# Optimization experiments

Measured on AMD Instinct MI355X. Metric: run time of the kernel, lower is better.

## Reference

```python
import jax, jax.numpy as jnp
import numpy as np

T, D, R, C, L = 4096, 512, 32, 32, 2  # time, input, trace, context, num_blocks
NEG_SLOPE = 0.01
EPS = 1e-5  # eqx LayerNorm default


def _layernorm(x, g, b):
    m = jnp.mean(x, -1, keepdims=True)
    v = jnp.var(x, -1, keepdims=True)
    return g * (x - m) * jax.lax.rsqrt(v + EPS) + b


def _ffa_scan(a, b, pre, s0, start):
    # a:[R], b:[C], pre:[T,R,C] real>=0, s0:[1,R,C] complex64, start:[T] bool
    ab = jax.lax.complex(jnp.broadcast_to(-jnp.abs(a)[:, None], (R, C)),
                         jnp.broadcast_to(b[None, :], (R, C)))  # log decay+rotation
    ts = jnp.concatenate([jnp.zeros((1,), jnp.float32), jnp.ones((T,), jnp.float32)])
    vals = jnp.concatenate([s0, pre.astype(jnp.complex64)], axis=0)  # [T+1,R,C]
    rst = jnp.concatenate([jnp.zeros((1,), bool), start])

    def op(l, r):
        tl, sl, dl = l
        tr, sr, dr = r
        decay = jnp.exp(ab[None, :, :] * tr[:, None, None])  # gamma^{t_r}
        s = jnp.where(dr[:, None, None], sr, sr + sl * decay)
        t = jnp.where(dr, tr, tl + tr)
        return (t, s, dl | dr)

    _, states, _ = jax.lax.associative_scan(op, (ts, vals, rst))
    return states[1:]  # [T,R,C]


def _forward(x, start_b, state_real, state_imag, Wt, Wc, a, b,
             W0, b0, g0, beta0, W1, b1, g1, beta1):
    h = x
    z = x
    for i in range(L):
        tr = h @ Wt[i].T  # [T,R]
        ct = h @ Wc[i].T  # [T,R] (source maps context proj to trace_size too; R==C)
        pre = jnp.abs(tr[:, :, None] * ct[:, None, :])  # [T,R,C] outer product
        pre = pre / (1e-8 + jnp.sum(pre, axis=(-2, -1), keepdims=True))
        s0 = jax.lax.complex(state_real[i], state_imag[i])  # [1,R,C]
        states = _ffa_scan(a[i], b[i], pre, s0, start_b)
        s = states.reshape(T, R * C)
        mag = jnp.log1p(jnp.abs(s))
        ang = jnp.angle(s)
        scaled = jnp.concatenate([mag * jnp.sin(ang), mag * jnp.cos(ang)], axis=-1)  # [T,2RC]
        z = jax.nn.leaky_relu(_layernorm(scaled @ W0[i].T + b0[i], g0[i], beta0[i]), NEG_SLOPE)
        z = jax.nn.leaky_relu(_layernorm(z @ W1[i].T + b1[i], g1[i], beta1[i]), NEG_SLOPE)
        h = h + z  # residual feeds next block; NSFFM returns last block's z
    return z


def setup_inputs() -> dict:
    key = jax.random.key(0)
    ks = jax.random.split(key, 8)
    x = jax.random.normal(ks[0], (T, D), jnp.float32)
    start = jax.random.randint(ks[1], (T,), 0, 2).astype(jnp.int32)
    next_done = jax.random.randint(ks[2], (T,), 0, 2).astype(jnp.int32)
    Wt = jax.random.normal(ks[3], (L, R, D), jnp.float32) / np.sqrt(D)
    Wc = jax.random.normal(ks[4], (L, R, D), jnp.float32) / np.sqrt(D)
    # ffa.init: a = linspace decays, b = log-spaced angular frequencies
    a = jnp.broadcast_to(jnp.linspace(1e-6, 0.5, R, dtype=jnp.float32)[None], (L, R)).copy()
    b = jnp.broadcast_to((2 * jnp.pi / jnp.exp(jnp.linspace(np.log(1.0), np.log(1024.0), C))).astype(jnp.float32)[None], (L, C)).copy()
    W0 = jax.random.normal(ks[5], (L, D, 2 * R * C), jnp.float32) * 0.01  # default_init scale=0.01
    W1 = jax.random.normal(ks[6], (L, D, D), jnp.float32) / np.sqrt(D)
    return {
        'x': x, 'start': start, 'next_done': next_done,
        'state_real': jnp.zeros((L, 1, R, C), jnp.float32),
        'state_imag': jnp.zeros((L, 1, R, C), jnp.float32),
        'Wt': Wt, 'Wc': Wc, 'a': a, 'b': b,
        'W0': W0, 'b0': jnp.zeros((L, D), jnp.float32),
        'g0': jnp.ones((L, D), jnp.float32), 'beta0': jnp.zeros((L, D), jnp.float32),
        'W1': W1, 'b1': jnp.zeros((L, D), jnp.float32),
        'g1': jnp.ones((L, D), jnp.float32), 'beta1': jnp.zeros((L, D), jnp.float32),
    }


def reference(x, start, next_done, state_real, state_imag, Wt, Wc, a, b,
              W0, b0, g0, beta0, W1, b1, g1, beta1):
    del next_done  # not used in the scan math (kept for interface parity)
    start_b = start.astype(bool)
    return _forward(x, start_b, state_real, state_imag, Wt, Wc, a, b,
                    W0, b0, g0, beta0, W1, b1, g1, beta1)
```

## Files before the change

kernel.cpp:

```cpp
#include <hip/hip_runtime.h>
#include <math.h>

#define TT 4096
#define DD 512
#define RR 32
#define CC 32
#define RC 1024
#define LL 2
#define CHUNK 32
#define NCHUNK 128
#define NEG_SLOPE 0.01f
#define LN_EPS 1e-5f

typedef __attribute__((ext_vector_type(8))) __bf16 bf16x8;
typedef __attribute__((ext_vector_type(4))) float f32x4;

__device__ __forceinline__ unsigned short f2bf(float f) {
    unsigned int u = __builtin_bit_cast(unsigned int, f);
    u += 0x7fffu + ((u >> 16) & 1u);
    return (unsigned short)(u >> 16);
}

#define NX4  524288
#define NW04 524288
#define NW14 131072
#define NCV  (NX4 + NW04 + NW14)
#define NPK  16384
__global__ __launch_bounds__(256) void setup_kernel(const float4* __restrict__ x,
                                                    const float4* __restrict__ W0,
                                                    const float4* __restrict__ W1,
                                                    const float* __restrict__ Wt,
                                                    const float* __restrict__ Wc,
                                                    ushort4* __restrict__ xb,
                                                    ushort4* __restrict__ W0b,
                                                    ushort4* __restrict__ W1b,
                                                    ushort4* __restrict__ Wtc) {
    int i = blockIdx.x * 256 + threadIdx.x;
    float4 v;
    ushort4* dst;
    int j;
    if (i < NCV) {
        const float4* src;
        if (i < NX4) { src = x; dst = xb; j = i; }
        else if (i < NX4 + NW04) { src = W0; dst = W0b; j = i - NX4; }
        else { src = W1; dst = W1b; j = i - NX4 - NW04; }
        v = src[j];
    } else {
        int ii = i - NCV;
        if (ii >= NPK) return;
        int e = ii * 4;
        int l = e >> 15;
        int r = (e >> 9) & 63;
        int k = e & 511;
        v = (r < 32) ? *(const float4*)&Wt[((size_t)l * 32 + r) * 512 + k]
                     : *(const float4*)&Wc[((size_t)l * 32 + (r - 32)) * 512 + k];
        dst = Wtc; j = ii;
    }
    ushort4 o;
    o.x = f2bf(v.x); o.y = f2bf(v.y); o.z = f2bf(v.z); o.w = f2bf(v.w);
    dst[j] = o;
}

__global__ __launch_bounds__(256) void proj_denom_kernel(const unsigned short* __restrict__ A,
                                                         const unsigned short* __restrict__ B,
                                                         float* __restrict__ tcabs) {
    __shared__ __align__(16) unsigned short As[128 * 32];
    __shared__ __align__(16) unsigned short Bs[64 * 32];
    __shared__ float sums[128][2];
    const int tid = threadIdx.x;
    const int w = tid >> 6, lane = tid & 63;
    const int bm = blockIdx.y * 128;
    const int wr = w >> 1, wc = w & 1;
    const int lr = lane >> 2;
    const int sl = lane & 3;
    const int swz_st = sl ^ ((lr >> 1) & 3);
    const int K = 512;
    const unsigned short* gA0 = A + (size_t)(bm + w * 16 + lr) * K + sl * 8;
    const unsigned short* gA1 = A + (size_t)(bm + 64 + w * 16 + lr) * K + sl * 8;
    const unsigned short* gB  = B + (size_t)(w * 16 + lr) * K + sl * 8;
    const int wA0 = (w * 16 + lr) * 32 + swz_st * 8;
    const int wA1 = (64 + w * 16 + lr) * 32 + swz_st * 8;
    const int wB  = (w * 16 + lr) * 32 + swz_st * 8;
    const int fr = lane & 15, hi = lane >> 4;
    const int kslot = hi ^ ((fr >> 1) & 3);
    f32x4 acc[4][2] = {};

    uint4 va0 = *(const uint4*)gA0;
    uint4 va1 = *(const uint4*)gA1;
    uint4 vb  = *(const uint4*)gB;
    for (int k0 = 0; k0 < K; k0 += 32) {
        __syncthreads();
        *(uint4*)&As[wA0] = va0;
        *(uint4*)&As[wA1] = va1;
        *(uint4*)&Bs[wB]  = vb;
        __syncthreads();
        if (k0 + 32 < K) {
            va0 = *(const uint4*)(gA0 + k0 + 32);
            va1 = *(const uint4*)(gA1 + k0 + 32);
            vb  = *(const uint4*)(gB  + k0 + 32);
        }
        bf16x8 af[4], bfv[2];
#pragma unroll
        for (int mi = 0; mi < 4; ++mi) {
            int row = wr * 64 + mi * 16 + fr;
            af[mi] = *(const bf16x8*)&As[row * 32 + kslot * 8];
        }
#pragma unroll
        for (int ni = 0; ni < 2; ++ni) {
            int row = wc * 32 + ni * 16 + fr;
            bfv[ni] = *(const bf16x8*)&Bs[row * 32 + kslot * 8];
        }
#pragma unroll
        for (int mi = 0; mi < 4; ++mi)
#pragma unroll
            for (int ni = 0; ni < 2; ++ni)
                acc[mi][ni] = __builtin_amdgcn_mfma_f32_16x16x32_bf16(
                    af[mi], bfv[ni], acc[mi][ni], 0, 0, 0);
    }
#pragma unroll
    for (int mi = 0; mi < 4; ++mi)
#pragma unroll
        for (int q = 0; q < 4; ++q) {
            float v = fabsf(acc[mi][0][q]) + fabsf(acc[mi][1][q]);
            v += __shfl_xor(v, 1);
            v += __shfl_xor(v, 2);
            v += __shfl_xor(v, 4);
            v += __shfl_xor(v, 8);
            if (fr == 0) sums[wr * 64 + mi * 16 + hi * 4 + q][wc] = v;
        }
    __syncthreads();
#pragma unroll
    for (int mi = 0; mi < 4; ++mi)
#pragma unroll
        for (int q = 0; q < 4; ++q) {
            int rl = wr * 64 + mi * 16 + hi * 4 + q;
            float inv = 1.f / (1e-8f + sums[rl][0] * sums[rl][1]);
            float scale = (wc == 0) ? inv : 1.f;
#pragma unroll
            for (int ni = 0; ni < 2; ++ni) {
                int col = wc * 32 + ni * 16 + fr;
                tcabs[(size_t)(bm + rl) * 64 + col] = fabsf(acc[mi][ni][q]) * scale;
            }
        }
}

__global__ __launch_bounds__(256) void scan_pass1(const float* __restrict__ tcabs,
                                                  const int* __restrict__ start,
                                                  const float* __restrict__ a,
                                                  const float* __restrict__ b,
                                                  float4* __restrict__ ab4) {
    int tid = blockIdx.x * 256 + threadIdx.x;
    int rc = tid & (RC - 1);
    int chunk = tid >> 10;
    int r = rc >> 5, c = rc & 31;
    float e = expf(-fabsf(a[r]));
    float gr = e * cosf(b[c]);
    float gi = e * sinf(b[c]);
    float alr = 1.f, ali = 0.f, ber = 0.f, bei = 0.f;
    int t0 = chunk * CHUNK;
    for (int j = 0; j < CHUNK; ++j) {
        int t = t0 + j;
        float pre = tcabs[t * 64 + r] * tcabs[t * 64 + 32 + c];
        if (start[t]) {
            alr = 0.f; ali = 0.f; ber = pre; bei = 0.f;
        } else {
            float nbr = pre + gr * ber - gi * bei;
            float nbi =       gr * bei + gi * ber;
            float nar = gr * alr - gi * ali;
            float nai = gr * ali + gi * alr;
            ber = nbr; bei = nbi; alr = nar; ali = nai;
        }
    }
    ab4[chunk * RC + rc] = make_float4(alr, ali, ber, bei);
}

__global__ __launch_bounds__(256) void scan_pass2f(const float* __restrict__ tcabs,
                                                   const float4* __restrict__ ab4,
                                                   const int* __restrict__ start,
                                                   const float* __restrict__ a,
                                                   const float* __restrict__ b,
                                                   const float* __restrict__ s0r,
                                                   const float* __restrict__ s0i,
                                                   unsigned short* __restrict__ scaled) {
    int bx = blockIdx.x;
    int chunk = bx >> 2;
    int rc = (bx & 3) * 256 + threadIdx.x;
    int r = rc >> 5, c = rc & 31;
    float e = expf(-fabsf(a[r]));
    float gr = e * cosf(b[c]);
    float gi = e * sinf(b[c]);
    float sr = s0r[rc], si = s0i[rc];
    int j = 0;
    for (; j + 8 <= chunk; j += 8) {
        float4 buf[8];
#pragma unroll
        for (int u = 0; u < 8; ++u) buf[u] = ab4[(j + u) * RC + rc];
#pragma unroll
        for (int u = 0; u < 8; ++u) {
            float nsr = buf[u].z + buf[u].x * sr - buf[u].y * si;
            float nsi = buf[u].w + buf[u].x * si + buf[u].y * sr;
            sr = nsr; si = nsi;
        }
    }
    for (; j < chunk; ++j) {
        float4 ab = ab4[j * RC + rc];
        float nsr = ab.z + ab.x * sr - ab.y * si;
        float nsi = ab.w + ab.x * si + ab.y * sr;
        sr = nsr; si = nsi;
    }
    int t0 = chunk * CHUNK;
    for (int jj = 0; jj < CHUNK; ++jj) {
        int t = t0 + jj;
        float pre = tcabs[t * 64 + r] * tcabs[t * 64 + 32 + c];
        if (start[t]) {
            sr = pre; si = 0.f;
        } else {
            float nsr = pre + gr * sr - gi * si;
            float nsi =       gr * si + gi * sr;
            sr = nsr; si = nsi;
        }
        float m = sqrtf(sr * sr + si * si);
        float mag = log1pf(m);
        float f = (m > 0.f) ? (mag / m) : 0.f;
        scaled[(size_t)t * 2048 + rc]        = f2bf(si * f);
        scaled[(size_t)t * 2048 + 1024 + rc] = f2bf(sr * f);
    }
}

template <int K, int N, int SPLITK>
__global__ __launch_bounds__(256) void gemm_bt_mfma(const unsigned short* __restrict__ A,
                                                    const unsigned short* __restrict__ B,
                                                    float* __restrict__ Cm) {
    __shared__ __align__(16) unsigned short As[128 * 32];
    __shared__ __align__(16) unsigned short Bs[64 * 32];
    const int tid = threadIdx.x;
    const int w = tid >> 6, lane = tid & 63;
    const int bm = blockIdx.y * 128, bn = blockIdx.x * 64;
    const int kbeg = blockIdx.z * (K / SPLITK);
    const int kend = kbeg + (K / SPLITK);
    const int wr = w >> 1, wc = w & 1;
    const int lr = lane >> 2;
    const int sl = lane & 3;
    const int swz_st = sl ^ ((lr >> 1) & 3);
    const size_t a_row0 = (size_t)(bm + w * 16 + lr);
    const size_t a_row1 = (size_t)(bm + 64 + w * 16 + lr);
    const size_t b_row  = (size_t)(bn + w * 16 + lr);
    const unsigned short* gA0 = A + a_row0 * K + sl * 8;
    const unsigned short* gA1 = A + a_row1 * K + sl * 8;
    const unsigned short* gB  = B + b_row  * K + sl * 8;
    const int wA0 = (w * 16 + lr) * 32 + swz_st * 8;
    const int wA1 = (64 + w * 16 + lr) * 32 + swz_st * 8;
    const int wB  = (w * 16 + lr) * 32 + swz_st * 8;
    const int fr = lane & 15, hi = lane >> 4;
    const int kslot = hi ^ ((fr >> 1) & 3);
    f32x4 acc[4][2] = {};

    uint4 va0 = *(const uint4*)(gA0 + kbeg);
    uint4 va1 = *(const uint4*)(gA1 + kbeg);
    uint4 vb  = *(const uint4*)(gB  + kbeg);
    for (int k0 = kbeg; k0 < kend; k0 += 32) {
        __syncthreads();
        *(uint4*)&As[wA0] = va0;
        *(uint4*)&As[wA1] = va1;
        *(uint4*)&Bs[wB]  = vb;
        __syncthreads();
        if (k0 + 32 < kend) {
            va0 = *(const uint4*)(gA0 + k0 + 32);
            va1 = *(const uint4*)(gA1 + k0 + 32);
            vb  = *(const uint4*)(gB  + k0 + 32);
        }
        bf16x8 af[4], bfv[2];
#pragma unroll
        for (int mi = 0; mi < 4; ++mi) {
            int row = wr * 64 + mi * 16 + fr;
            af[mi] = *(const bf16x8*)&As[row * 32 + kslot * 8];
        }
#pragma unroll
        for (int ni = 0; ni < 2; ++ni) {
            int row = wc * 32 + ni * 16 + fr;
            bfv[ni] = *(const bf16x8*)&Bs[row * 32 + kslot * 8];
        }
#pragma unroll
        for (int mi = 0; mi < 4; ++mi)
#pragma unroll
            for (int ni = 0; ni < 2; ++ni)
                acc[mi][ni] = __builtin_amdgcn_mfma_f32_16x16x32_bf16(
                    af[mi], bfv[ni], acc[mi][ni], 0, 0, 0);
    }
    float* Cz = Cm + (size_t)blockIdx.z * TT * N;
    const int ccol0 = bn + wc * 32 + fr;
    const int crow0 = bm + wr * 64 + hi * 4;
#pragma unroll
    for (int ni = 0; ni < 2; ++ni) {
        int col = ccol0 + ni * 16;
#pragma unroll
        for (int mi = 0; mi < 4; ++mi)
#pragma unroll
            for (int q = 0; q < 4; ++q)
                Cz[(size_t)(crow0 + mi * 16 + q) * N + col] = acc[mi][ni][q];
    }
}

__global__ __launch_bounds__(256) void ln_lrelu_kernel(const float* __restrict__ y0,
                                                       const float* __restrict__ y1,
                                                       const float* __restrict__ badd,
                                                       const float* __restrict__ g,
                                                       const float* __restrict__ be,
                                                       unsigned short* __restrict__ zb,
                                                       const float* __restrict__ res,
                                                       unsigned short* __restrict__ hbf,
                                                       float* __restrict__ fout) {
    int t = blockIdx.x;
    int tid = threadIdx.x;
    size_t base = (size_t)t * 512;
    float v0 = y0[base + tid] + y1[base + tid] + badd[tid];
    float v1 = y0[base + 256 + tid] + y1[base + 256 + tid] + badd[256 + tid];
    float s = v0 + v1, ss = v0 * v0 + v1 * v1;
#pragma unroll
    for (int o = 32; o > 0; o >>= 1) {
        s  += __shfl_down(s, o);
        ss += __shfl_down(ss, o);
    }
    __shared__ float sh[8];
    __shared__ float mrs[2];
    int wid = tid >> 6, lane = tid & 63;
    if (lane == 0) { sh[wid] = s; sh[4 + wid] = ss; }
    __syncthreads();
    if (tid == 0) {
        float S = sh[0] + sh[1] + sh[2] + sh[3];
        float SS = sh[4] + sh[5] + sh[6] + sh[7];
        float m = S * (1.f / 512.f);
        float var = SS * (1.f / 512.f) - m * m;
        mrs[0] = m;
        mrs[1] = rsqrtf(var + LN_EPS);
    }
    __syncthreads();
    float m = mrs[0], rs = mrs[1];
    float z0 = g[tid] * (v0 - m) * rs + be[tid];
    float z1 = g[256 + tid] * (v1 - m) * rs + be[256 + tid];
    z0 = (z0 > 0.f) ? z0 : NEG_SLOPE * z0;
    z1 = (z1 > 0.f) ? z1 : NEG_SLOPE * z1;
    if (zb)   { zb[base + tid] = f2bf(z0); zb[base + 256 + tid] = f2bf(z1); }
    if (hbf) {
        float h0 = (res ? res[base + tid] : 0.f) + z0;
        float h1 = (res ? res[base + 256 + tid] : 0.f) + z1;
        hbf[base + tid] = f2bf(h0);
        hbf[base + 256 + tid] = f2bf(h1);
    }
    if (fout) { fout[base + tid] = z0; fout[base + 256 + tid] = z1; }
}

extern "C" void kernel_launch(void* const* d_in, const int* in_sizes, int n_in,
                              void* d_out, int out_size, void* d_ws, size_t ws_size,
                              hipStream_t stream) {
    const float* x     = (const float*)d_in[0];
    const int*   start = (const int*)d_in[1];
    const float* s0r = (const float*)d_in[3];
    const float* s0i = (const float*)d_in[4];
    const float* Wt  = (const float*)d_in[5];
    const float* Wc  = (const float*)d_in[6];
    const float* a   = (const float*)d_in[7];
    const float* b   = (const float*)d_in[8];
    const float* W0  = (const float*)d_in[9];
    const float* b0  = (const float*)d_in[10];
    const float* g0  = (const float*)d_in[11];
    const float* be0 = (const float*)d_in[12];
    const float* W1  = (const float*)d_in[13];
    const float* b1  = (const float*)d_in[14];
    const float* g1  = (const float*)d_in[15];
    const float* be1 = (const float*)d_in[16];
    float* out = (float*)d_out;
    float* ws  = (float*)d_ws;

    float* p = ws;
    float* tcabs  = p; p += 262144;
    float4* ab4   = (float4*)p; p += 524288;
    unsigned short* scaled = (unsigned short*)p; p += 4194304;
    float* ybufp  = p; p += 4194304;
    unsigned short* zbuf_bf = (unsigned short*)p; p += 1048576;
    unsigned short* x_bf    = (unsigned short*)p; p += 1048576;
    unsigned short* h_bf    = (unsigned short*)p; p += 1048576;
    unsigned short* Wtcbf   = (unsigned short*)p; p += 32768;
    unsigned short* W0bf    = (unsigned short*)p; p += 1048576;
    unsigned short* W1bf    = (unsigned short*)p; p += 262144;

    setup_kernel<<<(NCV + NPK + 255) / 256, 256, 0, stream>>>(
        (const float4*)x, (const float4*)W0, (const float4*)W1, Wt, Wc,
        (ushort4*)x_bf, (ushort4*)W0bf, (ushort4*)W1bf, (ushort4*)Wtcbf);

    for (int i = 0; i < LL; ++i) {
        const unsigned short* hb = (i == 0) ? x_bf : h_bf;
        proj_denom_kernel<<<dim3(1, 32), 256, 0, stream>>>(
            hb, Wtcbf + (size_t)i * 64 * 512, tcabs);
        scan_pass1<<<NCHUNK * RC / 256, 256, 0, stream>>>(
            tcabs, start, a + i * RR, b + i * CC, ab4);
        scan_pass2f<<<NCHUNK * 4, 256, 0, stream>>>(
            tcabs, ab4, start, a + i * RR, b + i * CC,
            s0r + i * RC, s0i + i * RC, scaled);
        gemm_bt_mfma<2048, 512, 2><<<dim3(8, 32, 2), 256, 0, stream>>>(
            scaled, W0bf + (size_t)i * 512 * 2048, ybufp);
        ln_lrelu_kernel<<<TT, 256, 0, stream>>>(
            ybufp, ybufp + (size_t)TT * 512, b0 + i * DD, g0 + i * DD, be0 + i * DD,
            zbuf_bf, nullptr, nullptr, nullptr);
        gemm_bt_mfma<512, 512, 2><<<dim3(8, 32, 2), 256, 0, stream>>>(
            zbuf_bf, W1bf + (size_t)i * 512 * 512, ybufp);
        ln_lrelu_kernel<<<TT, 256, 0, stream>>>(
            ybufp, ybufp + (size_t)TT * 512, b1 + i * DD, g1 + i * DD, be1 + i * DD,
            nullptr,
            (i < LL - 1) ? x : nullptr,
            (i < LL - 1) ? h_bf : nullptr,
            (i == LL - 1) ? out : nullptr);
    }
}
```

Baseline: 208.9 us.

## Retile projection kernel to 64-row blocks and remap GEMM workgroups across XCDs

The projection/denominator kernel now uses 64-row tiles with each wave owning 16 full rows, so it launches 64 workgroups instead of 32. The row normalizer is computed with in-wave shuffles alone, which removes the shared-memory sums array and an extra barrier. The main GEMM now remaps its linear workgroup id so that consecutive tiles land on the same XCD (8-way interleave), meant to improve L2 reuse of shared A/B tiles. This assumes the workgroup count is divisible by 8, and each wave in the projection kernel does less reuse of its A fragment.

```diff
diff --git a/kernel.cpp b/kernel.cpp
--- a/kernel.cpp
+++ b/kernel.cpp
@@ -64,84 +64,61 @@
 __global__ __launch_bounds__(256) void proj_denom_kernel(const unsigned short* __restrict__ A,
                                                          const unsigned short* __restrict__ B,
                                                          float* __restrict__ tcabs) {
-    __shared__ __align__(16) unsigned short As[128 * 32];
+    __shared__ __align__(16) unsigned short As[64 * 32];
     __shared__ __align__(16) unsigned short Bs[64 * 32];
-    __shared__ float sums[128][2];
     const int tid = threadIdx.x;
     const int w = tid >> 6, lane = tid & 63;
-    const int bm = blockIdx.y * 128;
-    const int wr = w >> 1, wc = w & 1;
-    const int lr = lane >> 2;
-    const int sl = lane & 3;
-    const int swz_st = sl ^ ((lr >> 1) & 3);
+    const int bm = blockIdx.x * 64;
     const int K = 512;
-    const unsigned short* gA0 = A + (size_t)(bm + w * 16 + lr) * K + sl * 8;
-    const unsigned short* gA1 = A + (size_t)(bm + 64 + w * 16 + lr) * K + sl * 8;
-    const unsigned short* gB  = B + (size_t)(w * 16 + lr) * K + sl * 8;
-    const int wA0 = (w * 16 + lr) * 32 + swz_st * 8;
-    const int wA1 = (64 + w * 16 + lr) * 32 + swz_st * 8;
-    const int wB  = (w * 16 + lr) * 32 + swz_st * 8;
+    const int srow = tid >> 2;
+    const int sl = tid & 3;
+    const int sswz = (sl ^ ((srow >> 1) & 3)) * 8;
+    const unsigned short* gA = A + (size_t)(bm + srow) * K + sl * 8;
+    const unsigned short* gB = B + (size_t)srow * K + sl * 8;
+    const int wA = srow * 32 + sswz;
+    const int wB = srow * 32 + sswz;
     const int fr = lane & 15, hi = lane >> 4;
     const int kslot = hi ^ ((fr >> 1) & 3);
-    f32x4 acc[4][2] = {};
-
-    uint4 va0 = *(const uint4*)gA0;
-    uint4 va1 = *(const uint4*)gA1;
-    uint4 vb  = *(const uint4*)gB;
+    f32x4 acc0 = {}, acc1 = {}, acc2 = {}, acc3 = {};
+
+    uint4 va = *(const uint4*)gA;
+    uint4 vb = *(const uint4*)gB;
     for (int k0 = 0; k0 < K; k0 += 32) {
         __syncthreads();
-        *(uint4*)&As[wA0] = va0;
-        *(uint4*)&As[wA1] = va1;
-        *(uint4*)&Bs[wB]  = vb;
+        *(uint4*)&As[wA] = va;
+        *(uint4*)&Bs[wB] = vb;
         __syncthreads();
         if (k0 + 32 < K) {
-            va0 = *(const uint4*)(gA0 + k0 + 32);
-            va1 = *(const uint4*)(gA1 + k0 + 32);
-            vb  = *(const uint4*)(gB  + k0 + 32);
-        }
-        bf16x8 af[4], bfv[2];
-#pragma unroll
-        for (int mi = 0; mi < 4; ++mi) {
-            int row = wr * 64 + mi * 16 + fr;
-            af[mi] = *(const bf16x8*)&As[row * 32 + kslot * 8];
-        }
-#pragma unroll
-        for (int ni = 0; ni < 2; ++ni) {
-            int row = wc * 32 + ni * 16 + fr;
-            bfv[ni] = *(const bf16x8*)&Bs[row * 32 + kslot * 8];
-        }
-#pragma unroll
-        for (int mi = 0; mi < 4; ++mi)
-#pragma unroll
-            for (int ni = 0; ni < 2; ++ni)
-                acc[mi][ni] = __builtin_amdgcn_mfma_f32_16x16x32_bf16(
-                    af[mi], bfv[ni], acc[mi][ni], 0, 0, 0);
-    }
-#pragma unroll
-    for (int mi = 0; mi < 4; ++mi)
-#pragma unroll
-        for (int q = 0; q < 4; ++q) {
-            float v = fabsf(acc[mi][0][q]) + fabsf(acc[mi][1][q]);
-            v += __shfl_xor(v, 1);
-            v += __shfl_xor(v, 2);
-            v += __shfl_xor(v, 4);
-            v += __shfl_xor(v, 8);
-            if (fr == 0) sums[wr * 64 + mi * 16 + hi * 4 + q][wc] = v;
-        }
-    __syncthreads();
-#pragma unroll
-    for (int mi = 0; mi < 4; ++mi)
-#pragma unroll
-        for (int q = 0; q < 4; ++q) {
-            int rl = wr * 64 + mi * 16 + hi * 4 + q;
-            float inv = 1.f / (1e-8f + sums[rl][0] * sums[rl][1]);
-            float scale = (wc == 0) ? inv : 1.f;
-#pragma unroll
-            for (int ni = 0; ni < 2; ++ni) {
-                int col = wc * 32 + ni * 16 + fr;
-                tcabs[(size_t)(bm + rl) * 64 + col] = fabsf(acc[mi][ni][q]) * scale;
-            }
-        }
+            va = *(const uint4*)(gA + k0 + 32);
+            vb = *(const uint4*)(gB + k0 + 32);
+        }
+        const int arow = w * 16 + fr;
+        bf16x8 af = *(const bf16x8*)&As[arow * 32 + kslot * 8];
+        bf16x8 b0 = *(const bf16x8*)&Bs[(0 * 16 + fr) * 32 + kslot * 8];
+        bf16x8 b1 = *(const bf16x8*)&Bs[(1 * 16 + fr) * 32 + kslot * 8];
+        bf16x8 b2 = *(const bf16x8*)&Bs[(2 * 16 + fr) * 32 + kslot * 8];
+        bf16x8 b3 = *(const bf16x8*)&Bs[(3 * 16 + fr) * 32 + kslot * 8];
+        acc0 = __builtin_amdgcn_mfma_f32_16x16x32_bf16(af, b0, acc0, 0, 0, 0);
+        acc1 = __builtin_amdgcn_mfma_f32_16x16x32_bf16(af, b1, acc1, 0, 0, 0);
+        acc2 = __builtin_amdgcn_mfma_f32_16x16x32_bf16(af, b2, acc2, 0, 0, 0);
+        acc3 = __builtin_amdgcn_mfma_f32_16x16x32_bf16(af, b3, acc3, 0, 0, 0);
+    }
+#pragma unroll
+    for (int q = 0; q < 4; ++q) {
+        float a0 = fabsf(acc0[q]), a1 = fabsf(acc1[q]);
+        float a2 = fabsf(acc2[q]), a3 = fabsf(acc3[q]);
+        float st = a0 + a1, sc = a2 + a3;
+        st += __shfl_xor(st, 1); sc += __shfl_xor(sc, 1);
+        st += __shfl_xor(st, 2); sc += __shfl_xor(sc, 2);
+        st += __shfl_xor(st, 4); sc += __shfl_xor(sc, 4);
+        st += __shfl_xor(st, 8); sc += __shfl_xor(sc, 8);
+        float inv = 1.f / (1e-8f + st * sc);
+        size_t rb = (size_t)(bm + w * 16 + hi * 4 + q) * 64;
+        tcabs[rb + fr]      = a0 * inv;
+        tcabs[rb + fr + 16] = a1 * inv;
+        tcabs[rb + fr + 32] = a2;
+        tcabs[rb + fr + 48] = a3;
+    }
 }
 
 __global__ __launch_bounds__(256) void scan_pass1(const float* __restrict__ tcabs,
@@ -235,8 +212,15 @@
     __shared__ __align__(16) unsigned short Bs[64 * 32];
     const int tid = threadIdx.x;
     const int w = tid >> 6, lane = tid & 63;
-    const int bm = blockIdx.y * 128, bn = blockIdx.x * 64;
-    const int kbeg = blockIdx.z * (K / SPLITK);
+    const int nwg = gridDim.x * gridDim.y * gridDim.z;
+    const int id = blockIdx.x + gridDim.x * (blockIdx.y + gridDim.y * blockIdx.z);
+    const int lid = (id & 7) * (nwg >> 3) + (id >> 3);
+    const int bxs = lid % gridDim.x;
+    const int t2 = lid / gridDim.x;
+    const int bys = t2 % gridDim.y;
+    const int bzs = t2 / gridDim.y;
+    const int bm = bys * 128, bn = bxs * 64;
+    const int kbeg = bzs * (K / SPLITK);
     const int kend = kbeg + (K / SPLITK);
     const int wr = w >> 1, wc = w & 1;
     const int lr = lane >> 2;
@@ -287,7 +271,7 @@
                 acc[mi][ni] = __builtin_amdgcn_mfma_f32_16x16x32_bf16(
                     af[mi], bfv[ni], acc[mi][ni], 0, 0, 0);
     }
-    float* Cz = Cm + (size_t)blockIdx.z * TT * N;
+    float* Cz = Cm + (size_t)bzs * TT * N;
     const int ccol0 = bn + wc * 32 + fr;
     const int crow0 = bm + wr * 64 + hi * 4;
 #pragma unroll
@@ -390,7 +374,7 @@
 
     for (int i = 0; i < LL; ++i) {
         const unsigned short* hb = (i == 0) ? x_bf : h_bf;
-        proj_denom_kernel<<<dim3(1, 32), 256, 0, stream>>>(
+        proj_denom_kernel<<<64, 256, 0, stream>>>(
             hb, Wtcbf + (size_t)i * 64 * 512, tcabs);
         scan_pass1<<<NCHUNK * RC / 256, 256, 0, stream>>>(
             tcabs, start, a + i * RR, b + i * CC, ab4);
```

After: 202.4 us. -3.1%, faster.
